# Kernel tuning notes

Hardware: AMD Instinct MI355X
Metric: run time of the kernel (lower is better)

The kernel has to match this reference:

```python
import jax, jax.numpy as jnp
import numpy as np
import math

N = 100000   # outputSize (memory bank rows)
D = 128      # inputSize (feature dim)
B = 128      # batch size
K = 4096     # number of negatives per sample
T = 0.07     # temperature
MOMENTUM = 0.5


def setup_inputs() -> dict:
    key = jax.random.key(0)
    k1, k2, k3, k4, k5 = jax.random.split(key, 5)
    stdv = 1.0 / math.sqrt(D / 3.0)
    # l2-normalized features, as produced by the encoder in contrastive setups
    v1 = jax.random.normal(k1, (B, D), dtype=jnp.float32)
    v1 = v1 / jnp.linalg.norm(v1, axis=1, keepdims=True)
    v2 = jax.random.normal(k2, (B, D), dtype=jnp.float32)
    v2 = v2 / jnp.linalg.norm(v2, axis=1, keepdims=True)
    idx = jax.random.randint(k3, (B, K + 1), 0, N, dtype=jnp.int32)  # pos+neg bank rows
    y = jnp.arange(B, dtype=jnp.int32)  # distinct positive slots (first-visit behavior)
    # memory buffers initialized U(-stdv, stdv), as in torch.rand*2*stdv - stdv
    memory_v1 = jax.random.uniform(k4, (N, D), dtype=jnp.float32, minval=-stdv, maxval=stdv)
    memory_v2 = jax.random.uniform(k5, (N, D), dtype=jnp.float32, minval=-stdv, maxval=stdv)
    return {"v1": v1, "v2": v2, "idx": idx, "y": y,
            "memory_v1": memory_v1, "memory_v2": memory_v2}


def reference(v1, v2, idx, y, memory_v1, memory_v2):
    n_out = memory_v1.shape[0]
    # gather K+1 rows per sample (detached in the original -> stop_gradient)
    w1 = jax.lax.stop_gradient(memory_v1[idx])  # [B, K+1, D]
    w2 = jax.lax.stop_gradient(memory_v2[idx])  # [B, K+1, D]
    # batched vector-matrix product + exp/T
    out_v2 = jnp.exp(jnp.einsum('bkd,bd->bk', w1, v2) / T)  # [B, K+1]
    out_v1 = jnp.exp(jnp.einsum('bkd,bd->bk', w2, v1) / T)  # [B, K+1]
    # normalization constants (first-call Z computation: mean * outputSize)
    Z_v1 = jax.lax.stop_gradient(out_v1.mean()) * n_out
    Z_v2 = jax.lax.stop_gradient(out_v2.mean()) * n_out
    out_v1 = out_v1 / Z_v1
    out_v2 = out_v2 / Z_v2
    # momentum-blended normalize-and-scatter memory update (no_grad in torch)
    upd1 = MOMENTUM * memory_v1[y] + (1.0 - MOMENTUM) * v1  # [B, D]
    upd1 = upd1 / jnp.linalg.norm(upd1, axis=1, keepdims=True)
    new_memory_v1 = memory_v1.at[y].set(upd1)
    upd2 = MOMENTUM * memory_v2[y] + (1.0 - MOMENTUM) * v2
    upd2 = upd2 / jnp.linalg.norm(upd2, axis=1, keepdims=True)
    new_memory_v2 = memory_v2.at[y].set(upd2)
    return out_v1, out_v2, new_memory_v1, new_memory_v2
```

## Files before the change

### kernel.cpp

```cpp
#include <hip/hip_runtime.h>
#include <math.h>

constexpr int N_ROWS = 100000;
constexpr int D      = 128;
constexpr int B      = 128;
constexpr int KP1    = 4097;
constexpr int TOTAL_PAIRS = B * KP1;
constexpr float INV_T = 1.0f / 0.07f;
constexpr int N4 = N_ROWS * (D / 4);

constexpr int SC_BLOCKS = 1024;
constexpr int CP_BLOCKS = 1024;

typedef float fvec4 __attribute__((ext_vector_type(4)));

__global__ void init_ws_kernel(float* ws) {
    if (threadIdx.x < 2) ws[threadIdx.x] = 0.0f;
}

__device__ __forceinline__ float dot4(float4 a, float4 b) {
    return a.x * b.x + a.y * b.y + a.z * b.z + a.w * b.w;
}

__device__ __forceinline__ float red32(float v) {
    #pragma unroll
    for (int off = 16; off >= 1; off >>= 1) v += __shfl_xor(v, off);
    return v;
}

__global__ __launch_bounds__(256) void mega_kernel(
    const float* __restrict__ v1, const float* __restrict__ v2,
    const int* __restrict__ idx,
    const float* __restrict__ mem1, const float* __restrict__ mem2,
    float* __restrict__ out,
    float* __restrict__ sums,
    float* __restrict__ o1, float* __restrict__ o2)
{
    if (blockIdx.x & 1) {
        int cid = blockIdx.x >> 1;
        const fvec4* __restrict__ m1 = (const fvec4*)mem1;
        const fvec4* __restrict__ m2 = (const fvec4*)mem2;
        fvec4* __restrict__ d1 = (fvec4*)o1;
        fvec4* __restrict__ d2 = (fvec4*)o2;
        int tid = cid * 256 + threadIdx.x;
        int stride = CP_BLOCKS * 256;
        for (int i = tid; i < N4; i += stride) {
            fvec4 x1 = m1[i];
            fvec4 x2 = m2[i];
            __builtin_nontemporal_store(x1, &d1[i]);
            __builtin_nontemporal_store(x2, &d2[i]);
        }
        return;
    }

    __shared__ alignas(16) int s_idx[516];
    __shared__ float s1[8], s2[8];

    const int sid   = blockIdx.x >> 1;
    const int tid   = threadIdx.x;
    const int l     = tid & 31;
    const int grp   = tid >> 5;
    const int b     = sid >> 3;
    const int chunk = sid & 7;
    const int cnt   = (chunk == 7) ? 513 : 512;
    const int ibase = b * KP1 + chunk * 512;

    for (int t = tid; t < cnt; t += 256) s_idx[t] = idx[ibase + t];
    __syncthreads();

    const float4* __restrict__ m1 = (const float4*)mem1;
    const float4* __restrict__ m2 = (const float4*)mem2;
    const float4 a1 = ((const float4*)v1)[b * 32 + l];
    const float4 a2 = ((const float4*)v2)[b * 32 + l];

    const int lk    = grp * 64;
    const int pbase = ibase + lk;

    float acc1 = 0.0f, acc2 = 0.0f;

    for (int u = 0; u < 64; u += 4) {
        const int4 rr = *(const int4*)&s_idx[lk + u];

        float4 wA0 = m2[(size_t)rr.x * 32 + l];
        float4 wB0 = m1[(size_t)rr.x * 32 + l];
        float4 wA1 = m2[(size_t)rr.y * 32 + l];
        float4 wB1 = m1[(size_t)rr.y * 32 + l];
        float4 wA2 = m2[(size_t)rr.z * 32 + l];
        float4 wB2 = m1[(size_t)rr.z * 32 + l];
        float4 wA3 = m2[(size_t)rr.w * 32 + l];
        float4 wB3 = m1[(size_t)rr.w * 32 + l];

        float dA0 = red32(dot4(wA0, a1));
        float dB0 = red32(dot4(wB0, a2));
        float dA1 = red32(dot4(wA1, a1));
        float dB1 = red32(dot4(wB1, a2));
        float dA2 = red32(dot4(wA2, a1));
        float dB2 = red32(dot4(wB2, a2));
        float dA3 = red32(dot4(wA3, a1));
        float dB3 = red32(dot4(wB3, a2));

        float eA0 = __expf(dA0 * INV_T);
        float eB0 = __expf(dB0 * INV_T);
        float eA1 = __expf(dA1 * INV_T);
        float eB1 = __expf(dB1 * INV_T);
        float eA2 = __expf(dA2 * INV_T);
        float eB2 = __expf(dB2 * INV_T);
        float eA3 = __expf(dA3 * INV_T);
        float eB3 = __expf(dB3 * INV_T);

        acc1 += (eA0 + eA1) + (eA2 + eA3);
        acc2 += (eB0 + eB1) + (eB2 + eB3);

        float sa  = (l & 1) ? eA1 : eA0;
        float sb  = (l & 1) ? eA3 : eA2;
        float evA = (l & 2) ? sb : sa;
        float sc  = (l & 1) ? eB1 : eB0;
        float sd  = (l & 1) ? eB3 : eB2;
        float evB = (l & 2) ? sd : sc;
        int p = pbase + u;
        if (l < 4)      out[p + l] = evA;
        else if (l < 8) out[TOTAL_PAIRS + p + (l - 4)] = evB;
    }

    if (chunk == 7 && grp == 7) {
        int r = s_idx[512];
        float4 wA = m2[(size_t)r * 32 + l];
        float4 wB = m1[(size_t)r * 32 + l];
        float dA = red32(dot4(wA, a1));
        float dB = red32(dot4(wB, a2));
        float eA = __expf(dA * INV_T);
        float eB = __expf(dB * INV_T);
        acc1 += eA;
        acc2 += eB;
        if (l == 0) {
            out[b * KP1 + 4096]               = eA;
            out[TOTAL_PAIRS + b * KP1 + 4096] = eB;
        }
    }

    if (l == 0) { s1[grp] = acc1; s2[grp] = acc2; }
    __syncthreads();
    if (tid == 0) {
        float t1 = 0.0f, t2 = 0.0f;
        #pragma unroll
        for (int i = 0; i < 8; ++i) { t1 += s1[i]; t2 += s2[i]; }
        atomicAdd(&sums[0], t1);
        atomicAdd(&sums[1], t2);
    }
}

__global__ __launch_bounds__(256) void finish_kernel(
    float* __restrict__ out, const float* __restrict__ sums,
    const float* __restrict__ v1, const float* __restrict__ v2,
    const int* __restrict__ y,
    const float* __restrict__ mem1, const float* __restrict__ mem2,
    float* __restrict__ o1, float* __restrict__ o2)
{
    if (blockIdx.x < 2 * B && threadIdx.x < 64) {
        int b    = blockIdx.x & (B - 1);
        int bank = blockIdx.x >> 7;
        int lane = threadIdx.x;
        const float2* __restrict__ m = (const float2*)(bank ? mem2 : mem1);
        const float2* __restrict__ v = (const float2*)(bank ? v2 : v1);
        float2* __restrict__ o       = (float2*)(bank ? o2 : o1);
        int row = y[b];
        float2 mv = m[(size_t)row * 64 + lane];
        float2 vv = v[b * 64 + lane];
        float2 u;
        u.x = 0.5f * mv.x + 0.5f * vv.x;
        u.y = 0.5f * mv.y + 0.5f * vv.y;
        float ss = u.x * u.x + u.y * u.y;
        #pragma unroll
        for (int off = 32; off >= 1; off >>= 1) ss += __shfl_xor(ss, off);
        float inv = 1.0f / sqrtf(ss);
        float2 r; r.x = u.x * inv; r.y = u.y * inv;
        o[(size_t)row * 64 + lane] = r;
    }

    float sc1 = (float)((double)TOTAL_PAIRS / ((double)sums[0] * (double)N_ROWS));
    float sc2 = (float)((double)TOTAL_PAIRS / ((double)sums[1] * (double)N_ROWS));
    int stride = gridDim.x * blockDim.x;
    for (int i = blockIdx.x * blockDim.x + threadIdx.x; i < 2 * TOTAL_PAIRS;
         i += stride) {
        out[i] *= (i < TOTAL_PAIRS) ? sc1 : sc2;
    }
}

extern "C" void kernel_launch(void* const* d_in, const int* in_sizes, int n_in,
                              void* d_out, int out_size, void* d_ws, size_t ws_size,
                              hipStream_t stream) {
    const float* v1   = (const float*)d_in[0];
    const float* v2   = (const float*)d_in[1];
    const int*   idx  = (const int*)d_in[2];
    const int*   y    = (const int*)d_in[3];
    const float* mem1 = (const float*)d_in[4];
    const float* mem2 = (const float*)d_in[5];

    float* out = (float*)d_out;
    float* out_mem1 = out + 2 * (size_t)TOTAL_PAIRS;
    float* out_mem2 = out_mem1 + (size_t)N_ROWS * D;
    float* sums = (float*)d_ws;

    init_ws_kernel<<<1, 64, 0, stream>>>(sums);

    mega_kernel<<<SC_BLOCKS + CP_BLOCKS, 256, 0, stream>>>(
        v1, v2, idx, mem1, mem2, out, sums, out_mem1, out_mem2);

    finish_kernel<<<1024, 256, 0, stream>>>(
        out, sums, v1, v2, y, mem1, mem2, out_mem1, out_mem2);
}
```

Before: 282.7 us.

## Split fused score/copy kernel into separate score, copy+scale, and row-update kernels

The interleaved gather-score and memory-copy blocks are split into separate kernels. The score kernel now uses 2048 blocks with half the indices per block, and the bank copy is fused with the output normalization scaling in a second kernel. A third small kernel does the momentum row update after the copy. This gives up overlap of the gather-heavy scoring with the streaming copy in exchange for simpler per-kernel scheduling and more parallelism in scoring.

```diff
diff --git a/kernel.cpp b/kernel.cpp
--- a/kernel.cpp
+++ b/kernel.cpp
@@ -9,8 +9,8 @@
 constexpr float INV_T = 1.0f / 0.07f;
 constexpr int N4 = N_ROWS * (D / 4);
 
-constexpr int SC_BLOCKS = 1024;
-constexpr int CP_BLOCKS = 1024;
+constexpr int SC_BLOCKS = 2048;
+constexpr int CP_BLOCKS = 2048;
 
 typedef float fvec4 __attribute__((ext_vector_type(4)));
 
@@ -28,42 +28,24 @@
     return v;
 }
 
-__global__ __launch_bounds__(256) void mega_kernel(
+__global__ __launch_bounds__(256) void score_kernel(
     const float* __restrict__ v1, const float* __restrict__ v2,
     const int* __restrict__ idx,
     const float* __restrict__ mem1, const float* __restrict__ mem2,
     float* __restrict__ out,
-    float* __restrict__ sums,
-    float* __restrict__ o1, float* __restrict__ o2)
+    float* __restrict__ sums)
 {
-    if (blockIdx.x & 1) {
-        int cid = blockIdx.x >> 1;
-        const fvec4* __restrict__ m1 = (const fvec4*)mem1;
-        const fvec4* __restrict__ m2 = (const fvec4*)mem2;
-        fvec4* __restrict__ d1 = (fvec4*)o1;
-        fvec4* __restrict__ d2 = (fvec4*)o2;
-        int tid = cid * 256 + threadIdx.x;
-        int stride = CP_BLOCKS * 256;
-        for (int i = tid; i < N4; i += stride) {
-            fvec4 x1 = m1[i];
-            fvec4 x2 = m2[i];
-            __builtin_nontemporal_store(x1, &d1[i]);
-            __builtin_nontemporal_store(x2, &d2[i]);
-        }
-        return;
-    }
-
-    __shared__ alignas(16) int s_idx[516];
+    __shared__ alignas(16) int s_idx[260];
     __shared__ float s1[8], s2[8];
 
-    const int sid   = blockIdx.x >> 1;
+    const int sid   = blockIdx.x;
     const int tid   = threadIdx.x;
     const int l     = tid & 31;
     const int grp   = tid >> 5;
-    const int b     = sid >> 3;
-    const int chunk = sid & 7;
-    const int cnt   = (chunk == 7) ? 513 : 512;
-    const int ibase = b * KP1 + chunk * 512;
+    const int b     = sid >> 4;
+    const int chunk = sid & 15;
+    const int cnt   = (chunk == 15) ? 257 : 256;
+    const int ibase = b * KP1 + chunk * 256;
 
     for (int t = tid; t < cnt; t += 256) s_idx[t] = idx[ibase + t];
     __syncthreads();
@@ -73,12 +55,12 @@
     const float4 a1 = ((const float4*)v1)[b * 32 + l];
     const float4 a2 = ((const float4*)v2)[b * 32 + l];
 
-    const int lk    = grp * 64;
+    const int lk    = grp * 32;
     const int pbase = ibase + lk;
 
     float acc1 = 0.0f, acc2 = 0.0f;
 
-    for (int u = 0; u < 64; u += 4) {
+    for (int u = 0; u < 32; u += 4) {
         const int4 rr = *(const int4*)&s_idx[lk + u];
 
         float4 wA0 = m2[(size_t)rr.x * 32 + l];
@@ -122,8 +104,8 @@
         else if (l < 8) out[TOTAL_PAIRS + p + (l - 4)] = evB;
     }
 
-    if (chunk == 7 && grp == 7) {
-        int r = s_idx[512];
+    if (chunk == 15 && grp == 7) {
+        int r = s_idx[256];
         float4 wA = m2[(size_t)r * 32 + l];
         float4 wB = m1[(size_t)r * 32 + l];
         float dA = red32(dot4(wA, a1));
@@ -149,41 +131,56 @@
     }
 }
 
-__global__ __launch_bounds__(256) void finish_kernel(
-    float* __restrict__ out, const float* __restrict__ sums,
+__global__ __launch_bounds__(256) void copy_scale_kernel(
+    const float* __restrict__ mem1, const float* __restrict__ mem2,
+    float* __restrict__ o1, float* __restrict__ o2,
+    float* __restrict__ out, const float* __restrict__ sums)
+{
+    const fvec4* __restrict__ m1 = (const fvec4*)mem1;
+    const fvec4* __restrict__ m2 = (const fvec4*)mem2;
+    fvec4* __restrict__ d1 = (fvec4*)o1;
+    fvec4* __restrict__ d2 = (fvec4*)o2;
+
+    int tid    = blockIdx.x * 256 + threadIdx.x;
+    int stride = CP_BLOCKS * 256;
+    for (int i = tid; i < N4; i += stride) {
+        fvec4 x1 = m1[i];
+        fvec4 x2 = m2[i];
+        __builtin_nontemporal_store(x1, &d1[i]);
+        __builtin_nontemporal_store(x2, &d2[i]);
+    }
+
+    float sc1 = (float)((double)TOTAL_PAIRS / ((double)sums[0] * (double)N_ROWS));
+    float sc2 = (float)((double)TOTAL_PAIRS / ((double)sums[1] * (double)N_ROWS));
+    for (int i = tid; i < 2 * TOTAL_PAIRS; i += stride) {
+        out[i] *= (i < TOTAL_PAIRS) ? sc1 : sc2;
+    }
+}
+
+__global__ void rowupd_kernel(
     const float* __restrict__ v1, const float* __restrict__ v2,
     const int* __restrict__ y,
     const float* __restrict__ mem1, const float* __restrict__ mem2,
     float* __restrict__ o1, float* __restrict__ o2)
 {
-    if (blockIdx.x < 2 * B && threadIdx.x < 64) {
-        int b    = blockIdx.x & (B - 1);
-        int bank = blockIdx.x >> 7;
-        int lane = threadIdx.x;
-        const float2* __restrict__ m = (const float2*)(bank ? mem2 : mem1);
-        const float2* __restrict__ v = (const float2*)(bank ? v2 : v1);
-        float2* __restrict__ o       = (float2*)(bank ? o2 : o1);
-        int row = y[b];
-        float2 mv = m[(size_t)row * 64 + lane];
-        float2 vv = v[b * 64 + lane];
-        float2 u;
-        u.x = 0.5f * mv.x + 0.5f * vv.x;
-        u.y = 0.5f * mv.y + 0.5f * vv.y;
-        float ss = u.x * u.x + u.y * u.y;
-        #pragma unroll
-        for (int off = 32; off >= 1; off >>= 1) ss += __shfl_xor(ss, off);
-        float inv = 1.0f / sqrtf(ss);
-        float2 r; r.x = u.x * inv; r.y = u.y * inv;
-        o[(size_t)row * 64 + lane] = r;
-    }
-
-    float sc1 = (float)((double)TOTAL_PAIRS / ((double)sums[0] * (double)N_ROWS));
-    float sc2 = (float)((double)TOTAL_PAIRS / ((double)sums[1] * (double)N_ROWS));
-    int stride = gridDim.x * blockDim.x;
-    for (int i = blockIdx.x * blockDim.x + threadIdx.x; i < 2 * TOTAL_PAIRS;
-         i += stride) {
-        out[i] *= (i < TOTAL_PAIRS) ? sc1 : sc2;
-    }
+    int b    = blockIdx.x & (B - 1);
+    int bank = blockIdx.x >> 7;
+    int lane = threadIdx.x;
+    const float2* __restrict__ m = (const float2*)(bank ? mem2 : mem1);
+    const float2* __restrict__ v = (const float2*)(bank ? v2 : v1);
+    float2* __restrict__ o       = (float2*)(bank ? o2 : o1);
+    int row = y[b];
+    float2 mv = m[(size_t)row * 64 + lane];
+    float2 vv = v[b * 64 + lane];
+    float2 u;
+    u.x = 0.5f * mv.x + 0.5f * vv.x;
+    u.y = 0.5f * mv.y + 0.5f * vv.y;
+    float ss = u.x * u.x + u.y * u.y;
+    #pragma unroll
+    for (int off = 32; off >= 1; off >>= 1) ss += __shfl_xor(ss, off);
+    float inv = 1.0f / sqrtf(ss);
+    float2 r; r.x = u.x * inv; r.y = u.y * inv;
+    o[(size_t)row * 64 + lane] = r;
 }
 
 extern "C" void kernel_launch(void* const* d_in, const int* in_sizes, int n_in,
@@ -203,9 +200,12 @@
 
     init_ws_kernel<<<1, 64, 0, stream>>>(sums);
 
-    mega_kernel<<<SC_BLOCKS + CP_BLOCKS, 256, 0, stream>>>(
-        v1, v2, idx, mem1, mem2, out, sums, out_mem1, out_mem2);
-
-    finish_kernel<<<1024, 256, 0, stream>>>(
-        out, sums, v1, v2, y, mem1, mem2, out_mem1, out_mem2);
-}
+    score_kernel<<<SC_BLOCKS, 256, 0, stream>>>(
+        v1, v2, idx, mem1, mem2, out, sums);
+
+    copy_scale_kernel<<<CP_BLOCKS, 256, 0, stream>>>(
+        mem1, mem2, out_mem1, out_mem2, out, sums);
+
+    rowupd_kernel<<<2 * B, 64, 0, stream>>>(
+        v1, v2, y, mem1, mem2, out_mem1, out_mem2);
+}
```

Result: no change. 286.8 us (+1.4%).
